# Kernel optimization log

Hardware: AMD Instinct MI355X
Metric: run time of the kernel (lower is better)

Reference implementation:

```python
import jax, jax.numpy as jnp
import numpy as np

B = 4096      # number of boards
H = 256       # n_hidden
SCALE = 0.0625  # 1/sqrt(H)
N_POLICY = 1858


def setup_inputs() -> dict:
    key = jax.random.key(0)
    ks = jax.random.split(key, 10)
    w_s = 1.0 / 16.0  # keep activations well-scaled
    return {
        "x": jax.random.normal(ks[0], (B * 64, H), jnp.float32),
        "w1": jax.random.normal(ks[1], (H, H), jnp.float32) * w_s,
        "b1": jax.random.normal(ks[2], (H,), jnp.float32) * w_s,
        "w2": jax.random.normal(ks[3], (H, H), jnp.float32) * w_s,
        "b2": jax.random.normal(ks[4], (H,), jnp.float32) * w_s,
        "w3": jax.random.normal(ks[5], (H, H), jnp.float32) * w_s,
        "b3": jax.random.normal(ks[6], (H,), jnp.float32) * w_s,
        "w4": jax.random.normal(ks[7], (4, H), jnp.float32) * w_s,
        "gather_idx": jax.random.randint(ks[8], (N_POLICY,), 0, 4288, jnp.int32),
    }


def reference(x, w1, b1, w2, b2, w3, b3, w4, gather_idx):
    out = jax.nn.relu(x @ w1.T + b1)                      # (B*64, H)
    q = (out @ w2.T + b2).reshape(-1, 64, H)              # (B, 64, H)
    k = (out @ w3.T + b3).reshape(-1, 64, H)              # (B, 64, H)
    logits = jnp.einsum("bqh,bkh->bqk", q, k) * SCALE     # (B, 64, 64)

    # promotion offsets from 8th-rank keys
    promo_keys = k[:, 56:64, :]                           # (B, 8, H)
    offs = jnp.einsum("bsh,ph->bps", promo_keys, w4)      # (B, 4, 8)
    offs = offs[:, :3, :] + offs[:, 3:4, :]               # (B, 3, 8) q/r/b + knight base
    off24 = jnp.transpose(offs, (0, 2, 1)).reshape(-1, 1, 24)  # (B,1,24) piece-fastest

    # knight promotion move logits: rank7 -> rank8 block
    n_promo = logits[:, 48:56, 56:64].reshape(-1, 64, 1)  # (B, 64, 1)
    n_promo = jnp.broadcast_to(n_promo, (n_promo.shape[0], 64, 3)).reshape(-1, 8, 24)

    promo = (off24 + n_promo).reshape(-1, 3, 64)          # (B, 3, 64)

    full = jnp.concatenate([logits, promo], axis=1).reshape(-1, 4288)  # (B, 4288)
    return jnp.take(full, gather_idx, axis=1)             # (B, 1858)
```

## Files before the change

### kernel.cpp

```cpp
#include <hip/hip_runtime.h>


typedef __bf16 bf16_t;
typedef __bf16 bf16x8 __attribute__((ext_vector_type(8)));
typedef float  f32x4  __attribute__((ext_vector_type(4)));

#define PSCALE 0.0625f
#define NPOL   1858
#define MFMA(a,b,c) __builtin_amdgcn_mfma_f32_16x16x32_bf16(a, b, c, 0, 0, 0)


__global__ void prep_w1(const float* __restrict__ w1, bf16_t* __restrict__ wfA) {
    int i = blockIdx.x * 256 + threadIdx.x;
    int j = i & 7, lane = (i >> 3) & 63, t = (i >> 9) & 7, n = (i >> 12) & 15;
    int row = n * 16 + (lane & 15);
    int col = t * 32 + (lane >> 4) * 8 + j;
    wfA[i] = (bf16_t)w1[row * 256 + col];
}

__global__ void prep_mat(const float* __restrict__ w2,
                         const float* __restrict__ w3,
                         bf16_t* __restrict__ wfM) {
    int m1 = blockIdx.x, m2 = threadIdx.x;
    float acc = 0.f;
    #pragma unroll 8
    for (int h = 0; h < 256; ++h)
        acc += w2[h * 256 + m1] * w3[h * 256 + m2];
    int t = m1 >> 5, quad = (m1 >> 3) & 3, j = m1 & 7;
    int n = m2 >> 4, l15 = m2 & 15;
    wfM[(((n * 8 + t) * 64) + (quad * 16 + l15)) * 8 + j] = (bf16_t)acc;
}

__global__ void prep_vecs(const float* __restrict__ w2,
                          const float* __restrict__ w3,
                          const float* __restrict__ b2,
                          const float* __restrict__ b3,
                          const float* __restrict__ w4,
                          float* __restrict__ flt) {
    int m = threadIdx.x;
    float c2 = 0.f, vv = 0.f, p0 = 0.f, p1 = 0.f, p2 = 0.f, p3 = 0.f;
    for (int h = 0; h < 256; ++h) {
        float w3h = w3[h * 256 + m];
        c2 += b2[h] * w3h;
        p0 += w4[h] * w3h;
        p1 += w4[256 + h] * w3h;
        p2 += w4[512 + h] * w3h;
        p3 += w4[768 + h] * w3h;
        vv += w2[h * 256 + m] * b3[h];
    }
    flt[m]        = c2;
    flt[256 + m]  = vv;
    flt[512 + m]  = p0;
    flt[768 + m]  = p1;
    flt[1024 + m] = p2;
    flt[1280 + m] = p3;
    if (m < 4) {
        float pb = 0.f;
        for (int h = 0; h < 256; ++h) pb += w4[m * 256 + h] * b3[h];
        flt[1536 + m] = pb;
    }
    if (m == 0) {
        float s = 0.f;
        for (int h = 0; h < 256; ++h) s += b2[h] * b3[h];
        flt[1540] = s;
    }
}


template <bool USE_WS>
__device__ __forceinline__ bf16x8 wfrag(const bf16_t* __restrict__ wl,
                                        const float* __restrict__ w,
                                        int n, int t, int lane) {
    if constexpr (USE_WS) {
        return *(const bf16x8*)(wl + (((n * 8 + t) * 64 + lane) << 3));
    } else {
        int l15 = lane & 15, quad = lane >> 4;
        const float* p = w + (n * 16 + l15) * 256 + t * 32 + quad * 8;
        f32x4 lo = *(const f32x4*)p;
        f32x4 hi = *(const f32x4*)(p + 4);
        bf16x8 v;
        v[0] = (bf16_t)lo[0]; v[1] = (bf16_t)lo[1];
        v[2] = (bf16_t)lo[2]; v[3] = (bf16_t)lo[3];
        v[4] = (bf16_t)hi[0]; v[5] = (bf16_t)hi[1];
        v[6] = (bf16_t)hi[2]; v[7] = (bf16_t)hi[3];
        return v;
    }
}

__device__ __forceinline__ int ks_off(int row, int col) {
    return ((row << 9) + (col << 1)) ^ ((row & 7) << 4);
}

__device__ __forceinline__ bf16x8 cvt8(const float* __restrict__ p) {
    f32x4 lo = *(const f32x4*)p;
    f32x4 hi = *(const f32x4*)(p + 4);
    bf16x8 v;
    v[0] = (bf16_t)lo[0]; v[1] = (bf16_t)lo[1];
    v[2] = (bf16_t)lo[2]; v[3] = (bf16_t)lo[3];
    v[4] = (bf16_t)hi[0]; v[5] = (bf16_t)hi[1];
    v[6] = (bf16_t)hi[2]; v[7] = (bf16_t)hi[3];
    return v;
}

template <bool USE_WS, bool RELU>
__device__ __forceinline__ void layer2b(const bf16x8* inA, const bf16x8* inB,
                                        const bf16_t* __restrict__ wl,
                                        const float* __restrict__ wraw,
                                        const float* __restrict__ bias,
                                        unsigned char* __restrict__ u_lds,
                                        int lane, int quad, int l15, int R) {
    bf16x8 wA[4], wB[4];
    #pragma unroll
    for (int t = 0; t < 4; ++t)
        wA[t] = wfrag<USE_WS>(wl, wraw, 0, t, lane);

    #pragma unroll
    for (int n = 0; n < 16; ++n) {
        #pragma unroll
        for (int t = 0; t < 4; ++t)
            wB[t] = wfrag<USE_WS>(wl, wraw, n, 4 + t, lane);

        f32x4 aA0 = {0.f,0.f,0.f,0.f}, aA1 = {0.f,0.f,0.f,0.f};
        f32x4 aB0 = {0.f,0.f,0.f,0.f}, aB1 = {0.f,0.f,0.f,0.f};
        aA0 = MFMA(inA[0], wA[0], aA0);  aB0 = MFMA(inB[0], wA[0], aB0);
        aA1 = MFMA(inA[1], wA[1], aA1);  aB1 = MFMA(inB[1], wA[1], aB1);
        aA0 = MFMA(inA[2], wA[2], aA0);  aB0 = MFMA(inB[2], wA[2], aB0);
        aA1 = MFMA(inA[3], wA[3], aA1);  aB1 = MFMA(inB[3], wA[3], aB1);

        if (n < 15) {
            #pragma unroll
            for (int t = 0; t < 4; ++t)
                wA[t] = wfrag<USE_WS>(wl, wraw, n + 1, t, lane);
        }

        aA0 = MFMA(inA[4], wB[0], aA0);  aB0 = MFMA(inB[4], wB[0], aB0);
        aA1 = MFMA(inA[5], wB[1], aA1);  aB1 = MFMA(inB[5], wB[1], aB1);
        aA0 = MFMA(inA[6], wB[2], aA0);  aB0 = MFMA(inB[6], wB[2], aB0);
        aA1 = MFMA(inA[7], wB[3], aA1);  aB1 = MFMA(inB[7], wB[3], aB1);

        f32x4 sA = aA0 + aA1, sB = aB0 + aB1;
        float bv = bias[n * 16 + l15];
        #pragma unroll
        for (int r2 = 0; r2 < 4; ++r2) {
            int off = ks_off(R + quad * 4 + r2, n * 16 + l15);
            float vA = sA[r2] + bv, vB = sB[r2] + bv;
            if (RELU) { vA = fmaxf(vA, 0.f); vB = fmaxf(vB, 0.f); }
            *(bf16_t*)(u_lds + off)         = (bf16_t)vA;
            *(bf16_t*)(u_lds + 32768 + off) = (bf16_t)vB;
        }
    }
}

__global__ __launch_bounds__(256, 2)
void policy_fused(const float* __restrict__ x,
                  const bf16_t* __restrict__ wfA,
                  const bf16_t* __restrict__ wfM,
                  const float* __restrict__ flt,
                  const float* __restrict__ b1,
                  const int*   __restrict__ gidx,
                  float* __restrict__ out,
                  int nbat) {
    __shared__ __align__(16) unsigned char u_lds[2 * 32768];
    __shared__ __align__(16) bf16_t qscr[4][2][16 * 40];
    __shared__ float promoLDS[2][4][8];
    __shared__ float patchLDS[2][8][8];

    const int tid  = threadIdx.x;
    const int lane = tid & 63;
    const int wv   = tid >> 6;
    const int quad = lane >> 4;
    const int l15  = lane & 15;
    const int R    = wv * 16;

    const int bat0 = blockIdx.x * 2;
    const bool has1 = (bat0 + 1) < nbat;
    const int bat1 = has1 ? bat0 + 1 : bat0;

    bf16x8 xaA[8], xaB[8];
    {
        const float* xr0 = x + ((size_t)bat0 * 64 + R + l15) * 256;
        const float* xr1 = x + ((size_t)bat1 * 64 + R + l15) * 256;
        #pragma unroll
        for (int t = 0; t < 8; ++t) {
            xaA[t] = cvt8(xr0 + t * 32 + quad * 8);
            xaB[t] = cvt8(xr1 + t * 32 + quad * 8);
        }
    }

    layer2b<true, true>(xaA, xaB, wfA, nullptr, b1, u_lds, lane, quad, l15, R);
    bf16x8 oaA[8], oaB[8];
    #pragma unroll
    for (int t = 0; t < 8; ++t) {
        int off = ks_off(R + l15, t * 32 + quad * 8);
        oaA[t] = *(const bf16x8*)(u_lds + off);
        oaB[t] = *(const bf16x8*)(u_lds + 32768 + off);
    }

    float qbA = flt[1540], qbB = qbA;
    {
        const float* vvec = flt + 256;
        #pragma unroll
        for (int t = 0; t < 8; ++t) {
            f32x4 va = *(const f32x4*)(vvec + t * 32 + quad * 8);
            f32x4 vb = *(const f32x4*)(vvec + t * 32 + quad * 8 + 4);
            qbA += (float)oaA[t][0]*va[0] + (float)oaA[t][1]*va[1]
                 + (float)oaA[t][2]*va[2] + (float)oaA[t][3]*va[3]
                 + (float)oaA[t][4]*vb[0] + (float)oaA[t][5]*vb[1]
                 + (float)oaA[t][6]*vb[2] + (float)oaA[t][7]*vb[3];
            qbB += (float)oaB[t][0]*va[0] + (float)oaB[t][1]*va[1]
                 + (float)oaB[t][2]*va[2] + (float)oaB[t][3]*va[3]
                 + (float)oaB[t][4]*vb[0] + (float)oaB[t][5]*vb[1]
                 + (float)oaB[t][6]*vb[2] + (float)oaB[t][7]*vb[3];
        }
        qbA += __shfl_xor(qbA, 16);  qbA += __shfl_xor(qbA, 32);
        qbB += __shfl_xor(qbB, 16);  qbB += __shfl_xor(qbB, 32);
    }

    __syncthreads();

    f32x4 laA[4], laB[4];
    #pragma unroll
    for (int n = 0; n < 4; ++n) {
        laA[n] = (f32x4){0.f,0.f,0.f,0.f};
        laB[n] = (f32x4){0.f,0.f,0.f,0.f};
    }
    {
        bf16_t* qsA = &qscr[wv][0][0];
        bf16_t* qsB = &qscr[wv][1][0];
        bf16x8 wA[4], wB[4];
        #pragma unroll
        for (int t = 0; t < 4; ++t)
            wA[t] = wfrag<true>(wfM, nullptr, 0, t, lane);

        #pragma unroll
        for (int t8 = 0; t8 < 8; ++t8) {
            const int n0 = 2 * t8, n1 = n0 + 1;

            #pragma unroll
            for (int t = 0; t < 4; ++t)
                wB[t] = wfrag<true>(wfM, nullptr, n0, 4 + t, lane);
            {
                f32x4 cA0 = {0.f,0.f,0.f,0.f}, cA1 = {0.f,0.f,0.f,0.f};
                f32x4 cB0 = {0.f,0.f,0.f,0.f}, cB1 = {0.f,0.f,0.f,0.f};
                cA0 = MFMA(oaA[0], wA[0], cA0);  cB0 = MFMA(oaB[0], wA[0], cB0);
                cA1 = MFMA(oaA[1], wA[1], cA1);  cB1 = MFMA(oaB[1], wA[1], cB1);
                cA0 = MFMA(oaA[2], wA[2], cA0);  cB0 = MFMA(oaB[2], wA[2], cB0);
                cA1 = MFMA(oaA[3], wA[3], cA1);  cB1 = MFMA(oaB[3], wA[3], cB1);
                #pragma unroll
                for (int t = 0; t < 4; ++t)
                    wA[t] = wfrag<true>(wfM, nullptr, n1, t, lane);
                cA0 = MFMA(oaA[4], wB[0], cA0);  cB0 = MFMA(oaB[4], wB[0], cB0);
                cA1 = MFMA(oaA[5], wB[1], cA1);  cB1 = MFMA(oaB[5], wB[1], cB1);
                cA0 = MFMA(oaA[6], wB[2], cA0);  cB0 = MFMA(oaB[6], wB[2], cB0);
                cA1 = MFMA(oaA[7], wB[3], cA1);  cB1 = MFMA(oaB[7], wB[3], cB1);
                f32x4 sA = cA0 + cA1, sB = cB0 + cB1;
                float bv = flt[n0 * 16 + l15];
                #pragma unroll
                for (int r2 = 0; r2 < 4; ++r2) {
                    int qo = (quad * 4 + r2) * 40 + l15;
                    qsA[qo] = (bf16_t)(sA[r2] + bv);
                    qsB[qo] = (bf16_t)(sB[r2] + bv);
                }
            }

            #pragma unroll
            for (int t = 0; t < 4; ++t)
                wB[t] = wfrag<true>(wfM, nullptr, n1, 4 + t, lane);
            {
                f32x4 cA0 = {0.f,0.f,0.f,0.f}, cA1 = {0.f,0.f,0.f,0.f};
                f32x4 cB0 = {0.f,0.f,0.f,0.f}, cB1 = {0.f,0.f,0.f,0.f};
                cA0 = MFMA(oaA[0], wA[0], cA0);  cB0 = MFMA(oaB[0], wA[0], cB0);
                cA1 = MFMA(oaA[1], wA[1], cA1);  cB1 = MFMA(oaB[1], wA[1], cB1);
                cA0 = MFMA(oaA[2], wA[2], cA0);  cB0 = MFMA(oaB[2], wA[2], cB0);
                cA1 = MFMA(oaA[3], wA[3], cA1);  cB1 = MFMA(oaB[3], wA[3], cB1);
                if (t8 < 7) {
                    #pragma unroll
                    for (int t = 0; t < 4; ++t)
                        wA[t] = wfrag<true>(wfM, nullptr, n0 + 2, t, lane);
                }
                cA0 = MFMA(oaA[4], wB[0], cA0);  cB0 = MFMA(oaB[4], wB[0], cB0);
                cA1 = MFMA(oaA[5], wB[1], cA1);  cB1 = MFMA(oaB[5], wB[1], cB1);
                cA0 = MFMA(oaA[6], wB[2], cA0);  cB0 = MFMA(oaB[6], wB[2], cB0);
                cA1 = MFMA(oaA[7], wB[3], cA1);  cB1 = MFMA(oaB[7], wB[3], cB1);
                f32x4 sA = cA0 + cA1, sB = cB0 + cB1;
                float bv = flt[n1 * 16 + l15];
                #pragma unroll
                for (int r2 = 0; r2 < 4; ++r2) {
                    int qo = (quad * 4 + r2) * 40 + 16 + l15;
                    qsA[qo] = (bf16_t)(sA[r2] + bv);
                    qsB[qo] = (bf16_t)(sB[r2] + bv);
                }
            }

            bf16x8 qaA = *(const bf16x8*)(qsA + l15 * 40 + quad * 8);
            bf16x8 qaB = *(const bf16x8*)(qsB + l15 * 40 + quad * 8);
            #pragma unroll
            for (int np = 0; np < 4; ++np) {
                int ko = ks_off(np * 16 + l15, t8 * 32 + quad * 8);
                bf16x8 kA = *(const bf16x8*)(u_lds + ko);
                bf16x8 kB = *(const bf16x8*)(u_lds + 32768 + ko);
                laA[np] = MFMA(qaA, kA, laA[np]);
                laB[np] = MFMA(qaB, kB, laB[np]);
            }
        }
    }

    float qbra[4], qbrb[4];
    #pragma unroll
    for (int r2 = 0; r2 < 4; ++r2) {
        qbra[r2] = __shfl(qbA, quad * 4 + r2);
        qbrb[r2] = __shfl(qbB, quad * 4 + r2);
    }

    {
        int s = lane >> 3, seg = lane & 7;
        const float* wrow = flt + 512 + wv * 256;
        #pragma unroll
        for (int b = 0; b < 2; ++b) {
            const unsigned char* kb = u_lds + b * 32768;
            float p = 0.f;
            #pragma unroll
            for (int m = 0; m < 4; ++m) {
                bf16x8 kv = *(const bf16x8*)(kb + ks_off(56 + s, seg * 32 + m * 8));
                f32x4 wa = *(const f32x4*)(wrow + seg * 32 + m * 8);
                f32x4 wb = *(const f32x4*)(wrow + seg * 32 + m * 8 + 4);
                p += (float)kv[0] * wa[0] + (float)kv[1] * wa[1]
                   + (float)kv[2] * wa[2] + (float)kv[3] * wa[3]
                   + (float)kv[4] * wb[0] + (float)kv[5] * wb[1]
                   + (float)kv[6] * wb[2] + (float)kv[7] * wb[3];
            }
            p += __shfl_down(p, 4);
            p += __shfl_down(p, 2);
            p += __shfl_down(p, 1);
            if (seg == 0) promoLDS[b][wv][s] = p + flt[1536 + wv];
        }
    }

    if (wv == 3 && quad < 2 && l15 >= 8) {
        #pragma unroll
        for (int r2 = 0; r2 < 4; ++r2) {
            patchLDS[0][quad * 4 + r2][l15 - 8] = (laA[3][r2] + qbra[r2]) * PSCALE;
            patchLDS[1][quad * 4 + r2][l15 - 8] = (laB[3][r2] + qbrb[r2]) * PSCALE;
        }
    }

    __syncthreads();

    float* fb0 = (float*)u_lds;
    float* fb1 = (float*)(u_lds + 32768);
    #pragma unroll
    for (int n = 0; n < 4; ++n) {
        #pragma unroll
        for (int r2 = 0; r2 < 4; ++r2) {
            int idx = (R + quad * 4 + r2) * 64 + n * 16 + l15;
            fb0[idx] = (laA[n][r2] + qbra[r2]) * PSCALE;
            fb1[idx] = (laB[n][r2] + qbrb[r2]) * PSCALE;
        }
    }

    if (tid < 192) {
        int u = tid >> 6, vv2 = tid & 63;
        int mm = u * 64 + vv2;
        int r_ = mm / 24, c_ = mm - r_ * 24;
        int c3 = c_ / 3, cp = c_ - c3 * 3;
        fb0[(64 + u) * 64 + vv2] =
            promoLDS[0][cp][c3] + promoLDS[0][3][c3] + patchLDS[0][r_][c3];
        fb1[(64 + u) * 64 + vv2] =
            promoLDS[1][cp][c3] + promoLDS[1][3][c3] + patchLDS[1][r_][c3];
    }

    __syncthreads();

    {
        float* orow0 = out + (size_t)bat0 * NPOL;
        float* orow1 = out + (size_t)(bat0 + 1) * NPOL;
        int   idxv[8];
        float v0[8], v1[8];
        #pragma unroll
        for (int i = 0; i < 8; ++i) {
            int g = tid + i * 256;
            idxv[i] = (g < NPOL) ? gidx[g] : 0;
        }
        #pragma unroll
        for (int i = 0; i < 8; ++i) {
            v0[i] = fb0[idxv[i]];
            v1[i] = fb1[idxv[i]];
        }
        #pragma unroll
        for (int i = 0; i < 8; ++i) {
            int g = tid + i * 256;
            if (g < NPOL) {
                orow0[g] = v0[i];
                if (has1) orow1[g] = v1[i];
            }
        }
    }
}

template <bool USE_WS>
__global__ __launch_bounds__(256, 2)
void policy_main(const float* __restrict__ x,
                 const bf16_t* __restrict__ wf,
                 const float* __restrict__ w1,
                 const float* __restrict__ w2,
                 const float* __restrict__ w3,
                 const float* __restrict__ b1,
                 const float* __restrict__ b2,
                 const float* __restrict__ b3,
                 const float* __restrict__ w4,
                 const int*   __restrict__ gidx,
                 float* __restrict__ out,
                 int nbat) {
    __shared__ __align__(16) unsigned char u_lds[2 * 32768];
    __shared__ __align__(16) bf16_t qscr[4][2][16 * 40];
    __shared__ float promoLDS[2][4][8];
    __shared__ float patchLDS[2][8][8];

    const int tid  = threadIdx.x;
    const int lane = tid & 63;
    const int wv   = tid >> 6;
    const int quad = lane >> 4;
    const int l15  = lane & 15;
    const int R    = wv * 16;

    const int bat0 = blockIdx.x * 2;
    const bool has1 = (bat0 + 1) < nbat;
    const int bat1 = has1 ? bat0 + 1 : bat0;

    bf16x8 xaA[8], xaB[8];
    {
        const float* xr0 = x + ((size_t)bat0 * 64 + R + l15) * 256;
        const float* xr1 = x + ((size_t)bat1 * 64 + R + l15) * 256;
        #pragma unroll
        for (int t = 0; t < 8; ++t) {
            xaA[t] = cvt8(xr0 + t * 32 + quad * 8);
            xaB[t] = cvt8(xr1 + t * 32 + quad * 8);
        }
    }

    layer2b<USE_WS, true>(xaA, xaB, wf, w1, b1, u_lds, lane, quad, l15, R);
    bf16x8 oaA[8], oaB[8];
    #pragma unroll
    for (int t = 0; t < 8; ++t) {
        int off = ks_off(R + l15, t * 32 + quad * 8);
        oaA[t] = *(const bf16x8*)(u_lds + off);
        oaB[t] = *(const bf16x8*)(u_lds + 32768 + off);
    }

    layer2b<USE_WS, false>(oaA, oaB, wf + 2 * 65536, w3, b3, u_lds,
                           lane, quad, l15, R);

    __syncthreads();

    f32x4 laA[4], laB[4];
    #pragma unroll
    for (int n = 0; n < 4; ++n) {
        laA[n] = (f32x4){0.f,0.f,0.f,0.f};
        laB[n] = (f32x4){0.f,0.f,0.f,0.f};
    }
    {
        const bf16_t* wl = wf + 65536;
        bf16_t* qsA = &qscr[wv][0][0];
        bf16_t* qsB = &qscr[wv][1][0];
        bf16x8 wA[4], wB[4];
        #pragma unroll
        for (int t = 0; t < 4; ++t)
            wA[t] = wfrag<USE_WS>(wl, w2, 0, t, lane);

        #pragma unroll
        for (int t8 = 0; t8 < 8; ++t8) {
            const int n0 = 2 * t8, n1 = n0 + 1;
            #pragma unroll
            for (int t = 0; t < 4; ++t)
                wB[t] = wfrag<USE_WS>(wl, w2, n0, 4 + t, lane);
            {
                f32x4 cA0 = {0.f,0.f,0.f,0.f}, cA1 = {0.f,0.f,0.f,0.f};
                f32x4 cB0 = {0.f,0.f,0.f,0.f}, cB1 = {0.f,0.f,0.f,0.f};
                cA0 = MFMA(oaA[0], wA[0], cA0);  cB0 = MFMA(oaB[0], wA[0], cB0);
                cA1 = MFMA(oaA[1], wA[1], cA1);  cB1 = MFMA(oaB[1], wA[1], cB1);
                cA0 = MFMA(oaA[2], wA[2], cA0);  cB0 = MFMA(oaB[2], wA[2], cB0);
                cA1 = MFMA(oaA[3], wA[3], cA1);  cB1 = MFMA(oaB[3], wA[3], cB1);
                #pragma unroll
                for (int t = 0; t < 4; ++t)
                    wA[t] = wfrag<USE_WS>(wl, w2, n1, t, lane);
                cA0 = MFMA(oaA[4], wB[0], cA0);  cB0 = MFMA(oaB[4], wB[0], cB0);
                cA1 = MFMA(oaA[5], wB[1], cA1);  cB1 = MFMA(oaB[5], wB[1], cB1);
                cA0 = MFMA(oaA[6], wB[2], cA0);  cB0 = MFMA(oaB[6], wB[2], cB0);
                cA1 = MFMA(oaA[7], wB[3], cA1);  cB1 = MFMA(oaB[7], wB[3], cB1);
                f32x4 sA = cA0 + cA1, sB = cB0 + cB1;
                float bv = b2[n0 * 16 + l15];
                #pragma unroll
                for (int r2 = 0; r2 < 4; ++r2) {
                    int qo = (quad * 4 + r2) * 40 + l15;
                    qsA[qo] = (bf16_t)(sA[r2] + bv);
                    qsB[qo] = (bf16_t)(sB[r2] + bv);
                }
            }
            #pragma unroll
            for (int t = 0; t < 4; ++t)
                wB[t] = wfrag<USE_WS>(wl, w2, n1, 4 + t, lane);
            {
                f32x4 cA0 = {0.f,0.f,0.f,0.f}, cA1 = {0.f,0.f,0.f,0.f};
                f32x4 cB0 = {0.f,0.f,0.f,0.f}, cB1 = {0.f,0.f,0.f,0.f};
                cA0 = MFMA(oaA[0], wA[0], cA0);  cB0 = MFMA(oaB[0], wA[0], cB0);
                cA1 = MFMA(oaA[1], wA[1], cA1);  cB1 = MFMA(oaB[1], wA[1], cB1);
                cA0 = MFMA(oaA[2], wA[2], cA0);  cB0 = MFMA(oaB[2], wA[2], cB0);
                cA1 = MFMA(oaA[3], wA[3], cA1);  cB1 = MFMA(oaB[3], wA[3], cB1);
                if (t8 < 7) {
                    #pragma unroll
                    for (int t = 0; t < 4; ++t)
                        wA[t] = wfrag<USE_WS>(wl, w2, n0 + 2, t, lane);
                }
                cA0 = MFMA(oaA[4], wB[0], cA0);  cB0 = MFMA(oaB[4], wB[0], cB0);
                cA1 = MFMA(oaA[5], wB[1], cA1);  cB1 = MFMA(oaB[5], wB[1], cB1);
                cA0 = MFMA(oaA[6], wB[2], cA0);  cB0 = MFMA(oaB[6], wB[2], cB0);
                cA1 = MFMA(oaA[7], wB[3], cA1);  cB1 = MFMA(oaB[7], wB[3], cB1);
                f32x4 sA = cA0 + cA1, sB = cB0 + cB1;
                float bv = b2[n1 * 16 + l15];
                #pragma unroll
                for (int r2 = 0; r2 < 4; ++r2) {
                    int qo = (quad * 4 + r2) * 40 + 16 + l15;
                    qsA[qo] = (bf16_t)(sA[r2] + bv);
                    qsB[qo] = (bf16_t)(sB[r2] + bv);
                }
            }
            bf16x8 qaA = *(const bf16x8*)(qsA + l15 * 40 + quad * 8);
            bf16x8 qaB = *(const bf16x8*)(qsB + l15 * 40 + quad * 8);
            #pragma unroll
            for (int np = 0; np < 4; ++np) {
                int ko = ks_off(np * 16 + l15, t8 * 32 + quad * 8);
                bf16x8 kA = *(const bf16x8*)(u_lds + ko);
                bf16x8 kB = *(const bf16x8*)(u_lds + 32768 + ko);
                laA[np] = MFMA(qaA, kA, laA[np]);
                laB[np] = MFMA(qaB, kB, laB[np]);
            }
        }
    }

    {
        int s = lane >> 3, seg = lane & 7;
        const float* wrow = w4 + wv * 256;
        #pragma unroll
        for (int b = 0; b < 2; ++b) {
            const unsigned char* kb = u_lds + b * 32768;
            float p = 0.f;
            #pragma unroll
            for (int m = 0; m < 4; ++m) {
                bf16x8 kv = *(const bf16x8*)(kb + ks_off(56 + s, seg * 32 + m * 8));
                f32x4 wa = *(const f32x4*)(wrow + seg * 32 + m * 8);
                f32x4 wb = *(const f32x4*)(wrow + seg * 32 + m * 8 + 4);
                p += (float)kv[0] * wa[0] + (float)kv[1] * wa[1]
                   + (float)kv[2] * wa[2] + (float)kv[3] * wa[3]
                   + (float)kv[4] * wb[0] + (float)kv[5] * wb[1]
                   + (float)kv[6] * wb[2] + (float)kv[7] * wb[3];
            }
            p += __shfl_down(p, 4);
            p += __shfl_down(p, 2);
            p += __shfl_down(p, 1);
            if (seg == 0) promoLDS[b][wv][s] = p;
        }
    }

    if (wv == 3 && quad < 2 && l15 >= 8) {
        #pragma unroll
        for (int r2 = 0; r2 < 4; ++r2) {
            patchLDS[0][quad * 4 + r2][l15 - 8] = laA[3][r2] * PSCALE;
            patchLDS[1][quad * 4 + r2][l15 - 8] = laB[3][r2] * PSCALE;
        }
    }

    __syncthreads();

    float* fb0 = (float*)u_lds;
    float* fb1 = (float*)(u_lds + 32768);
    #pragma unroll
    for (int n = 0; n < 4; ++n) {
        #pragma unroll
        for (int r2 = 0; r2 < 4; ++r2) {
            int idx = (R + quad * 4 + r2) * 64 + n * 16 + l15;
            fb0[idx] = laA[n][r2] * PSCALE;
            fb1[idx] = laB[n][r2] * PSCALE;
        }
    }

    if (tid < 192) {
        int u = tid >> 6, vv2 = tid & 63;
        int mm = u * 64 + vv2;
        int r_ = mm / 24, c_ = mm - r_ * 24;
        int c3 = c_ / 3, cp = c_ - c3 * 3;
        fb0[(64 + u) * 64 + vv2] =
            promoLDS[0][cp][c3] + promoLDS[0][3][c3] + patchLDS[0][r_][c3];
        fb1[(64 + u) * 64 + vv2] =
            promoLDS[1][cp][c3] + promoLDS[1][3][c3] + patchLDS[1][r_][c3];
    }

    __syncthreads();

    {
        float* orow0 = out + (size_t)bat0 * NPOL;
        float* orow1 = out + (size_t)(bat0 + 1) * NPOL;
        int   idxv[8];
        float v0[8], v1[8];
        #pragma unroll
        for (int i = 0; i < 8; ++i) {
            int g = tid + i * 256;
            idxv[i] = (g < NPOL) ? gidx[g] : 0;
        }
        #pragma unroll
        for (int i = 0; i < 8; ++i) {
            v0[i] = fb0[idxv[i]];
            v1[i] = fb1[idxv[i]];
        }
        #pragma unroll
        for (int i = 0; i < 8; ++i) {
            int g = tid + i * 256;
            if (g < NPOL) {
                orow0[g] = v0[i];
                if (has1) orow1[g] = v1[i];
            }
        }
    }
}

extern "C" void kernel_launch(void* const* d_in, const int* in_sizes, int n_in,
                              void* d_out, int out_size, void* d_ws, size_t ws_size,
                              hipStream_t stream) {
    const float* x    = (const float*)d_in[0];
    const float* w1   = (const float*)d_in[1];
    const float* b1   = (const float*)d_in[2];
    const float* w2   = (const float*)d_in[3];
    const float* b2   = (const float*)d_in[4];
    const float* w3   = (const float*)d_in[5];
    const float* b3   = (const float*)d_in[6];
    const float* w4   = (const float*)d_in[7];
    const int*   gidx = (const int*)d_in[8];
    float* out = (float*)d_out;

    int nbat = in_sizes[0] / (64 * 256);
    int nblk = (nbat + 1) / 2;
    const size_t ws_needed = 262144 + 8192;

    if (ws_size >= ws_needed) {
        bf16_t* wfA = (bf16_t*)d_ws;
        bf16_t* wfM = wfA + 65536;
        float*  flt = (float*)((char*)d_ws + 262144);
        prep_w1  <<<256, 256, 0, stream>>>(w1, wfA);
        prep_mat <<<256, 256, 0, stream>>>(w2, w3, wfM);
        prep_vecs<<<1,   256, 0, stream>>>(w2, w3, b2, b3, w4, flt);
        policy_fused<<<nblk, 256, 0, stream>>>(
            x, wfA, wfM, flt, b1, gidx, out, nbat);
    } else {
        policy_main<false><<<nblk, 256, 0, stream>>>(
            x, nullptr, w1, w2, w3, b1, b2, b3, w4, gidx, out, nbat);
    }
}
```

Measured before the change: 501.4 us.

## Stage layer-1 weight fragments through LDS with async global-to-LDS double buffering

The first layer of the fused kernel no longer has each wave load its own W1 fragments from global memory into registers. Each wave now issues one global_load_lds of 1 KB per step into a double-buffered LDS staging area, and all waves share that slice. The loop runs in 32 half-steps with a __syncthreads each, so redundant global weight traffic is cut and register pressure drops, but 32 block barriers are added. The q scratch buffer is reused as the staging area, the next layer's first weight fragments are hoisted before the barrier, and the fallback path is refactored.

```diff
diff --git a/kernel.cpp b/kernel.cpp
--- a/kernel.cpp
+++ b/kernel.cpp
@@ -102,51 +102,59 @@
     return v;
 }
 
-template <bool USE_WS, bool RELU>
-__device__ __forceinline__ void layer2b(const bf16x8* inA, const bf16x8* inB,
-                                        const bf16_t* __restrict__ wl,
-                                        const float* __restrict__ wraw,
-                                        const float* __restrict__ bias,
-                                        unsigned char* __restrict__ u_lds,
-                                        int lane, int quad, int l15, int R) {
-    bf16x8 wA[4], wB[4];
-    #pragma unroll
-    for (int t = 0; t < 4; ++t)
-        wA[t] = wfrag<USE_WS>(wl, wraw, 0, t, lane);
-
-    #pragma unroll
-    for (int n = 0; n < 16; ++n) {
-        #pragma unroll
-        for (int t = 0; t < 4; ++t)
-            wB[t] = wfrag<USE_WS>(wl, wraw, n, 4 + t, lane);
-
-        f32x4 aA0 = {0.f,0.f,0.f,0.f}, aA1 = {0.f,0.f,0.f,0.f};
-        f32x4 aB0 = {0.f,0.f,0.f,0.f}, aB1 = {0.f,0.f,0.f,0.f};
-        aA0 = MFMA(inA[0], wA[0], aA0);  aB0 = MFMA(inB[0], wA[0], aB0);
-        aA1 = MFMA(inA[1], wA[1], aA1);  aB1 = MFMA(inB[1], wA[1], aB1);
-        aA0 = MFMA(inA[2], wA[2], aA0);  aB0 = MFMA(inB[2], wA[2], aB0);
-        aA1 = MFMA(inA[3], wA[3], aA1);  aB1 = MFMA(inB[3], wA[3], aB1);
-
-        if (n < 15) {
-            #pragma unroll
-            for (int t = 0; t < 4; ++t)
-                wA[t] = wfrag<USE_WS>(wl, wraw, n + 1, t, lane);
-        }
-
-        aA0 = MFMA(inA[4], wB[0], aA0);  aB0 = MFMA(inB[4], wB[0], aB0);
-        aA1 = MFMA(inA[5], wB[1], aA1);  aB1 = MFMA(inB[5], wB[1], aB1);
-        aA0 = MFMA(inA[6], wB[2], aA0);  aB0 = MFMA(inB[6], wB[2], aB0);
-        aA1 = MFMA(inA[7], wB[3], aA1);  aB1 = MFMA(inB[7], wB[3], aB1);
-
-        f32x4 sA = aA0 + aA1, sB = aB0 + aB1;
-        float bv = bias[n * 16 + l15];
-        #pragma unroll
-        for (int r2 = 0; r2 < 4; ++r2) {
-            int off = ks_off(R + quad * 4 + r2, n * 16 + l15);
-            float vA = sA[r2] + bv, vB = sB[r2] + bv;
-            if (RELU) { vA = fmaxf(vA, 0.f); vB = fmaxf(vB, 0.f); }
-            *(bf16_t*)(u_lds + off)         = (bf16_t)vA;
-            *(bf16_t*)(u_lds + 32768 + off) = (bf16_t)vB;
+__device__ __forceinline__ void gload_lds16(const void* g, void* l) {
+    __builtin_amdgcn_global_load_lds(
+        (const __attribute__((address_space(1))) void*)g,
+        (__attribute__((address_space(3))) void*)l, 16, 0, 0);
+}
+
+template <bool RELU>
+__device__ __forceinline__ void layer_staged(const bf16x8* inA, const bf16x8* inB,
+                                             const bf16_t* __restrict__ wsrc,
+                                             const float* __restrict__ bias,
+                                             unsigned char* __restrict__ u_lds,
+                                             unsigned char* __restrict__ wst,
+                                             int wv, int lane,
+                                             int quad, int l15, int R) {
+    const unsigned char* wsb = (const unsigned char*)wsrc;
+    gload_lds16(wsb + wv * 1024 + lane * 16, wst + wv * 1024);
+
+    f32x4 aA0, aA1, aB0, aB1;
+    #pragma unroll
+    for (int h = 0; h < 32; ++h) {
+        const int n = h >> 1, hb = h & 1;
+        __syncthreads();
+        if (h < 31) {
+            const int h1 = h + 1;
+            gload_lds16(wsb + (size_t)h1 * 4096 + wv * 1024 + lane * 16,
+                        wst + (h1 & 1) * 4096 + wv * 1024);
+        }
+        const unsigned char* sb = wst + (h & 1) * 4096;
+        bf16x8 w0 = *(const bf16x8*)(sb + 0 * 1024 + lane * 16);
+        bf16x8 w1 = *(const bf16x8*)(sb + 1 * 1024 + lane * 16);
+        bf16x8 w2 = *(const bf16x8*)(sb + 2 * 1024 + lane * 16);
+        bf16x8 w3 = *(const bf16x8*)(sb + 3 * 1024 + lane * 16);
+        if (hb == 0) {
+            aA0 = (f32x4){0.f,0.f,0.f,0.f}; aA1 = aA0;
+            aB0 = aA0; aB1 = aA0;
+        }
+        const bf16x8* iA = inA + hb * 4;
+        const bf16x8* iB = inB + hb * 4;
+        aA0 = MFMA(iA[0], w0, aA0);  aB0 = MFMA(iB[0], w0, aB0);
+        aA1 = MFMA(iA[1], w1, aA1);  aB1 = MFMA(iB[1], w1, aB1);
+        aA0 = MFMA(iA[2], w2, aA0);  aB0 = MFMA(iB[2], w2, aB0);
+        aA1 = MFMA(iA[3], w3, aA1);  aB1 = MFMA(iB[3], w3, aB1);
+        if (hb == 1) {
+            f32x4 sA = aA0 + aA1, sB = aB0 + aB1;
+            float bv = bias[n * 16 + l15];
+            #pragma unroll
+            for (int r2 = 0; r2 < 4; ++r2) {
+                int off = ks_off(R + quad * 4 + r2, n * 16 + l15);
+                float vA = sA[r2] + bv, vB = sB[r2] + bv;
+                if (RELU) { vA = fmaxf(vA, 0.f); vB = fmaxf(vB, 0.f); }
+                *(bf16_t*)(u_lds + off)         = (bf16_t)vA;
+                *(bf16_t*)(u_lds + 32768 + off) = (bf16_t)vB;
+            }
         }
     }
 }
@@ -161,7 +169,7 @@
                   float* __restrict__ out,
                   int nbat) {
     __shared__ __align__(16) unsigned char u_lds[2 * 32768];
-    __shared__ __align__(16) bf16_t qscr[4][2][16 * 40];
+    __shared__ __align__(16) unsigned char uq[10240];
     __shared__ float promoLDS[2][4][8];
     __shared__ float patchLDS[2][8][8];
 
@@ -187,7 +195,8 @@
         }
     }
 
-    layer2b<true, true>(xaA, xaB, wfA, nullptr, b1, u_lds, lane, quad, l15, R);
+    layer_staged<true>(xaA, xaB, wfA, b1, u_lds, uq, wv, lane, quad, l15, R);
+
     bf16x8 oaA[8], oaB[8];
     #pragma unroll
     for (int t = 0; t < 8; ++t) {
@@ -216,6 +225,11 @@
         qbB += __shfl_xor(qbB, 16);  qbB += __shfl_xor(qbB, 32);
     }
 
+    bf16x8 wA[4], wB[4];
+    #pragma unroll
+    for (int t = 0; t < 4; ++t)
+        wA[t] = wfrag<true>(wfM, nullptr, 0, t, lane);
+
     __syncthreads();
 
     f32x4 laA[4], laB[4];
@@ -225,12 +239,8 @@
         laB[n] = (f32x4){0.f,0.f,0.f,0.f};
     }
     {
-        bf16_t* qsA = &qscr[wv][0][0];
-        bf16_t* qsB = &qscr[wv][1][0];
-        bf16x8 wA[4], wB[4];
-        #pragma unroll
-        for (int t = 0; t < 4; ++t)
-            wA[t] = wfrag<true>(wfM, nullptr, 0, t, lane);
+        bf16_t* qsA = (bf16_t*)uq + (wv * 2 + 0) * 640;
+        bf16_t* qsB = (bf16_t*)uq + (wv * 2 + 1) * 640;
 
         #pragma unroll
         for (int t8 = 0; t8 < 8; ++t8) {
@@ -397,10 +407,66 @@
     }
 }
 
-template <bool USE_WS>
+__device__ __forceinline__ void mfma16f(const bf16x8* inA, const bf16x8* inB,
+                                        const bf16x8* w, f32x4& s0, f32x4& s1) {
+    f32x4 a00 = {0.f,0.f,0.f,0.f}, a01 = {0.f,0.f,0.f,0.f};
+    f32x4 a10 = {0.f,0.f,0.f,0.f}, a11 = {0.f,0.f,0.f,0.f};
+    #pragma unroll
+    for (int t = 0; t < 8; t += 2) {
+        a00 = MFMA(inA[t],     w[t],     a00);
+        a10 = MFMA(inB[t],     w[t],     a10);
+        a01 = MFMA(inA[t + 1], w[t + 1], a01);
+        a11 = MFMA(inB[t + 1], w[t + 1], a11);
+    }
+    s0 = a00 + a01;
+    s1 = a10 + a11;
+}
+
+template <bool RELU>
+__device__ __forceinline__ void layer_raw(const bf16x8* inA, const bf16x8* inB,
+                                          const float* __restrict__ wraw,
+                                          const float* __restrict__ bias,
+                                          unsigned char* __restrict__ u_lds,
+                                          int lane, int quad, int l15, int R) {
+    bf16x8 wA[4], wB[4];
+    #pragma unroll
+    for (int t = 0; t < 4; ++t)
+        wA[t] = wfrag<false>(nullptr, wraw, 0, t, lane);
+    #pragma unroll
+    for (int n = 0; n < 16; ++n) {
+        #pragma unroll
+        for (int t = 0; t < 4; ++t)
+            wB[t] = wfrag<false>(nullptr, wraw, n, 4 + t, lane);
+        f32x4 aA0 = {0.f,0.f,0.f,0.f}, aA1 = {0.f,0.f,0.f,0.f};
+        f32x4 aB0 = {0.f,0.f,0.f,0.f}, aB1 = {0.f,0.f,0.f,0.f};
+        aA0 = MFMA(inA[0], wA[0], aA0);  aB0 = MFMA(inB[0], wA[0], aB0);
+        aA1 = MFMA(inA[1], wA[1], aA1);  aB1 = MFMA(inB[1], wA[1], aB1);
+        aA0 = MFMA(inA[2], wA[2], aA0);  aB0 = MFMA(inB[2], wA[2], aB0);
+        aA1 = MFMA(inA[3], wA[3], aA1);  aB1 = MFMA(inB[3], wA[3], aB1);
+        if (n < 15) {
+            #pragma unroll
+            for (int t = 0; t < 4; ++t)
+                wA[t] = wfrag<false>(nullptr, wraw, n + 1, t, lane);
+        }
+        aA0 = MFMA(inA[4], wB[0], aA0);  aB0 = MFMA(inB[4], wB[0], aB0);
+        aA1 = MFMA(inA[5], wB[1], aA1);  aB1 = MFMA(inB[5], wB[1], aB1);
+        aA0 = MFMA(inA[6], wB[2], aA0);  aB0 = MFMA(inB[6], wB[2], aB0);
+        aA1 = MFMA(inA[7], wB[3], aA1);  aB1 = MFMA(inB[7], wB[3], aB1);
+        f32x4 sA = aA0 + aA1, sB = aB0 + aB1;
+        float bv = bias[n * 16 + l15];
+        #pragma unroll
+        for (int r2 = 0; r2 < 4; ++r2) {
+            int off = ks_off(R + quad * 4 + r2, n * 16 + l15);
+            float vA = sA[r2] + bv, vB = sB[r2] + bv;
+            if (RELU) { vA = fmaxf(vA, 0.f); vB = fmaxf(vB, 0.f); }
+            *(bf16_t*)(u_lds + off)         = (bf16_t)vA;
+            *(bf16_t*)(u_lds + 32768 + off) = (bf16_t)vB;
+        }
+    }
+}
+
 __global__ __launch_bounds__(256, 2)
 void policy_main(const float* __restrict__ x,
-                 const bf16_t* __restrict__ wf,
                  const float* __restrict__ w1,
                  const float* __restrict__ w2,
                  const float* __restrict__ w3,
@@ -438,7 +504,7 @@
         }
     }
 
-    layer2b<USE_WS, true>(xaA, xaB, wf, w1, b1, u_lds, lane, quad, l15, R);
+    layer_raw<true>(xaA, xaB, w1, b1, u_lds, lane, quad, l15, R);
     bf16x8 oaA[8], oaB[8];
     #pragma unroll
     for (int t = 0; t < 8; ++t) {
@@ -447,8 +513,7 @@
         oaB[t] = *(const bf16x8*)(u_lds + 32768 + off);
     }
 
-    layer2b<USE_WS, false>(oaA, oaB, wf + 2 * 65536, w3, b3, u_lds,
-                           lane, quad, l15, R);
+    layer_raw<false>(oaA, oaB, w3, b3, u_lds, lane, quad, l15, R);
 
     __syncthreads();
 
@@ -459,35 +524,24 @@
         laB[n] = (f32x4){0.f,0.f,0.f,0.f};
     }
     {
-        const bf16_t* wl = wf + 65536;
         bf16_t* qsA = &qscr[wv][0][0];
         bf16_t* qsB = &qscr[wv][1][0];
         bf16x8 wA[4], wB[4];
         #pragma unroll
         for (int t = 0; t < 4; ++t)
-            wA[t] = wfrag<USE_WS>(wl, w2, 0, t, lane);
+            wA[t] = wfrag<false>(nullptr, w2, 0, t, lane);
 
         #pragma unroll
         for (int t8 = 0; t8 < 8; ++t8) {
             const int n0 = 2 * t8, n1 = n0 + 1;
             #pragma unroll
             for (int t = 0; t < 4; ++t)
-                wB[t] = wfrag<USE_WS>(wl, w2, n0, 4 + t, lane);
+                wB[t] = wfrag<false>(nullptr, w2, n0, 4 + t, lane);
             {
-                f32x4 cA0 = {0.f,0.f,0.f,0.f}, cA1 = {0.f,0.f,0.f,0.f};
-                f32x4 cB0 = {0.f,0.f,0.f,0.f}, cB1 = {0.f,0.f,0.f,0.f};
-                cA0 = MFMA(oaA[0], wA[0], cA0);  cB0 = MFMA(oaB[0], wA[0], cB0);
-                cA1 = MFMA(oaA[1], wA[1], cA1);  cB1 = MFMA(oaB[1], wA[1], cB1);
-                cA0 = MFMA(oaA[2], wA[2], cA0);  cB0 = MFMA(oaB[2], wA[2], cB0);
-                cA1 = MFMA(oaA[3], wA[3], cA1);  cB1 = MFMA(oaB[3], wA[3], cB1);
-                #pragma unroll
-                for (int t = 0; t < 4; ++t)
-                    wA[t] = wfrag<USE_WS>(wl, w2, n1, t, lane);
-                cA0 = MFMA(oaA[4], wB[0], cA0);  cB0 = MFMA(oaB[4], wB[0], cB0);
-                cA1 = MFMA(oaA[5], wB[1], cA1);  cB1 = MFMA(oaB[5], wB[1], cB1);
-                cA0 = MFMA(oaA[6], wB[2], cA0);  cB0 = MFMA(oaB[6], wB[2], cB0);
-                cA1 = MFMA(oaA[7], wB[3], cA1);  cB1 = MFMA(oaB[7], wB[3], cB1);
-                f32x4 sA = cA0 + cA1, sB = cB0 + cB1;
+                f32x4 sA, sB;
+                bf16x8 wfull[8] = {wA[0], wA[1], wA[2], wA[3],
+                                   wB[0], wB[1], wB[2], wB[3]};
+                mfma16f(oaA, oaB, wfull, sA, sB);
                 float bv = b2[n0 * 16 + l15];
                 #pragma unroll
                 for (int r2 = 0; r2 < 4; ++r2) {
@@ -498,24 +552,15 @@
             }
             #pragma unroll
             for (int t = 0; t < 4; ++t)
-                wB[t] = wfrag<USE_WS>(wl, w2, n1, 4 + t, lane);
+                wA[t] = wfrag<false>(nullptr, w2, n1, t, lane);
+            #pragma unroll
+            for (int t = 0; t < 4; ++t)
+                wB[t] = wfrag<false>(nullptr, w2, n1, 4 + t, lane);
             {
-                f32x4 cA0 = {0.f,0.f,0.f,0.f}, cA1 = {0.f,0.f,0.f,0.f};
-                f32x4 cB0 = {0.f,0.f,0.f,0.f}, cB1 = {0.f,0.f,0.f,0.f};
-                cA0 = MFMA(oaA[0], wA[0], cA0);  cB0 = MFMA(oaB[0], wA[0], cB0);
-                cA1 = MFMA(oaA[1], wA[1], cA1);  cB1 = MFMA(oaB[1], wA[1], cB1);
-                cA0 = MFMA(oaA[2], wA[2], cA0);  cB0 = MFMA(oaB[2], wA[2], cB0);
-                cA1 = MFMA(oaA[3], wA[3], cA1);  cB1 = MFMA(oaB[3], wA[3], cB1);
-                if (t8 < 7) {
-                    #pragma unroll
-                    for (int t = 0; t < 4; ++t)
-                        wA[t] = wfrag<USE_WS>(wl, w2, n0 + 2, t, lane);
-                }
-                cA0 = MFMA(oaA[4], wB[0], cA0);  cB0 = MFMA(oaB[4], wB[0], cB0);
-                cA1 = MFMA(oaA[5], wB[1], cA1);  cB1 = MFMA(oaB[5], wB[1], cB1);
-                cA0 = MFMA(oaA[6], wB[2], cA0);  cB0 = MFMA(oaB[6], wB[2], cB0);
-                cA1 = MFMA(oaA[7], wB[3], cA1);  cB1 = MFMA(oaB[7], wB[3], cB1);
-                f32x4 sA = cA0 + cA1, sB = cB0 + cB1;
+                f32x4 sA, sB;
+                bf16x8 wfull[8] = {wA[0], wA[1], wA[2], wA[3],
+                                   wB[0], wB[1], wB[2], wB[3]};
+                mfma16f(oaA, oaB, wfull, sA, sB);
                 float bv = b2[n1 * 16 + l15];
                 #pragma unroll
                 for (int r2 = 0; r2 < 4; ++r2) {
@@ -523,6 +568,11 @@
                     qsA[qo] = (bf16_t)(sA[r2] + bv);
                     qsB[qo] = (bf16_t)(sB[r2] + bv);
                 }
+            }
+            if (t8 < 7) {
+                #pragma unroll
+                for (int t = 0; t < 4; ++t)
+                    wA[t] = wfrag<false>(nullptr, w2, n0 + 2, t, lane);
             }
             bf16x8 qaA = *(const bf16x8*)(qsA + l15 * 40 + quad * 8);
             bf16x8 qaB = *(const bf16x8*)(qsB + l15 * 40 + quad * 8);
@@ -650,7 +700,7 @@
         policy_fused<<<nblk, 256, 0, stream>>>(
             x, wfA, wfM, flt, b1, gidx, out, nbat);
     } else {
-        policy_main<false><<<nblk, 256, 0, stream>>>(
-            x, nullptr, w1, w2, w3, b1, b2, b3, w4, gidx, out, nbat);
-    }
-}
+        policy_main<<<nblk, 256, 0, stream>>>(
+            x, w1, w2, w3, b1, b2, b3, w4, gidx, out, nbat);
+    }
+}
```

After: 528.5 us. +5.4%, slower.
